# Kernel tuning notes

Hardware: AMD Instinct MI355X
Metric: run time of the kernel (lower is better)

## Reference

```python
import jax, jax.numpy as jnp
import numpy as np
from jax import lax

D_MODEL = 96
EXPAND = 2.66
D_INNER = int(EXPAND * D_MODEL)  # 255
DT_RANK = -(-D_MODEL // 16)      # 6
D_STATE = 8
K = 4                            # 4 scan directions
WIN = 8
NCLUST = 16
B, H, W = 2, 64, 64
N = H * W
L = 2 * N                        # opt/sar interleaved


def setup_inputs() -> dict:
    key = jax.random.key(0)
    ks = jax.random.split(key, 16)
    s = 0.05
    def rn(i, shape):
        return jax.random.normal(ks[i], shape, jnp.float32) * s
    # dt bias init: inv-softplus of dt ~ LogUniform[1e-3, 1e-1]
    dt = jnp.exp(jax.random.uniform(ks[10], (K, D_INNER)) * (np.log(0.1) - np.log(0.001)) + np.log(0.001))
    dt = jnp.clip(dt, 1e-4, None)
    inv_dt = dt + jnp.log(-jnp.expm1(-dt))
    A_logs = jnp.log(jnp.tile(jnp.arange(1, D_STATE + 1, dtype=jnp.float32)[None, :], (K * D_INNER, 1)))
    return dict(
        optical=jax.random.normal(ks[0], (B, D_MODEL, H, W), jnp.float32),
        sar=jax.random.normal(ks[1], (B, D_MODEL, H, W), jnp.float32),
        anchor_idx=jax.random.randint(ks[2], (B, NCLUST), 0, N),
        in_w_opt=rn(3, (2 * D_INNER, D_MODEL)),
        in_w_sar=rn(4, (2 * D_INNER, D_MODEL)),
        conv_w_opt=rn(5, (D_INNER, 1, 3, 3)),
        conv_b_opt=rn(6, (D_INNER,)),
        conv_w_sar=rn(7, (D_INNER, 1, 3, 3)),
        conv_b_sar=rn(8, (D_INNER,)),
        x_proj_weight=rn(9, (K, DT_RANK + 2 * D_STATE, D_INNER)),
        dt_projs_weight=rn(11, (K, D_INNER, DT_RANK)),
        dt_projs_bias=inv_dt.astype(jnp.float32),
        A_logs=A_logs,
        Ds=jnp.ones((K * D_INNER,), jnp.float32),
        ln_w_opt=jnp.ones((D_INNER,), jnp.float32),
        ln_b_opt=jnp.zeros((D_INNER,), jnp.float32),
        ln_w_sar=jnp.ones((D_INNER,), jnp.float32),
        ln_b_sar=jnp.zeros((D_INNER,), jnp.float32),
        out_w_opt=rn(12, (D_MODEL, D_INNER)),
        out_w_sar=rn(13, (D_MODEL, D_INNER)),
    )


def _dwconv(x, w, b):
    # depthwise 3x3, SAME padding; x: (B, D_INNER, H, W), w: (D_INNER, 1, 3, 3)
    y = lax.conv_general_dilated(x, w, (1, 1), [(1, 1), (1, 1)],
                                 dimension_numbers=('NCHW', 'OIHW', 'NCHW'),
                                 feature_group_count=D_INNER)
    return y + b[None, :, None, None]


def _ln(x, w, b):
    m = jnp.mean(x, -1, keepdims=True)
    v = jnp.mean((x - m) ** 2, -1, keepdims=True)
    return (x - m) * lax.rsqrt(v + 1e-5) * w + b


def _patches(x, order):
    # x: (B, C, H, W) -> (B, C, N) in one of 4 window-scan orders
    b, c, h, w_ = x.shape
    p = x.reshape(b, c, h // WIN, WIN, w_ // WIN, WIN)
    if order in ('ltr_utd', 'rtl_dtu'):
        p = p.transpose(0, 1, 2, 4, 3, 5)
    else:
        p = p.transpose(0, 1, 4, 2, 5, 3)
    if order in ('rtl_dtu', 'dtu_rtl'):
        p = jnp.flip(p, (2, 3, 4, 5))
    return p.reshape(b, c, -1)


def _selective_scan(u, delta, A, Bm, Cm, Ds2, bias):
    # u, delta: (B,K,C,L); A: (K,C,Ns); Bm, Cm: (B,K,Ns,L); Ds2, bias: (K,C)
    delta = jax.nn.softplus(delta + bias[None, :, :, None])
    u_l = jnp.moveaxis(u, 3, 0)      # (L,B,K,C)
    d_l = jnp.moveaxis(delta, 3, 0)
    B_l = jnp.moveaxis(Bm, 3, 0)     # (L,B,K,Ns)
    C_l = jnp.moveaxis(Cm, 3, 0)
    h0 = jnp.zeros(u.shape[:3] + (A.shape[-1],), u.dtype)  # (B,K,C,Ns)
    def step(h, inp):
        ut, dt, bt, ct = inp
        h = h * jnp.exp(dt[..., None] * A) + (dt * ut)[..., None] * bt[:, :, None, :]
        y = jnp.einsum('bkcn,bkn->bkc', h, ct)
        return h, y
    _, ys = lax.scan(step, h0, (u_l, d_l, B_l, C_l))
    return jnp.moveaxis(ys, 0, 3) + u * Ds2[None, :, :, None]


def _forward(optical, sar, in_w_opt, in_w_sar, conv_w_opt, conv_b_opt, conv_w_sar,
             conv_b_sar, x_proj_weight, dt_projs_weight, dt_projs_bias, A_logs, Ds,
             ln_w_opt, ln_b_opt, ln_w_sar, ln_b_sar, out_w_opt, out_w_sar, anchor_idx):
    C = D_INNER
    x_opt = optical.transpose(0, 2, 3, 1)  # (B,H,W,D_MODEL)
    x_sar = sar.transpose(0, 2, 3, 1)
    xo, zo = jnp.split(x_opt @ in_w_opt.T, 2, axis=-1)
    xs_, zs = jnp.split(x_sar @ in_w_sar.T, 2, axis=-1)
    xo = jax.nn.silu(_dwconv(xo.transpose(0, 3, 1, 2), conv_w_opt, conv_b_opt))   # (B,C,H,W)
    xs_ = jax.nn.silu(_dwconv(xs_.transpose(0, 3, 1, 2), conv_w_sar, conv_b_sar))
    # --- cluster-sorted token reorder ---
    xof = xo.reshape(B, C, N).transpose(0, 2, 1)   # (B,N,C)
    xsf = xs_.reshape(B, C, N).transpose(0, 2, 1)
    anchors = jnp.take_along_axis(xof, jnp.broadcast_to(anchor_idx[:, :, None], (B, NCLUST, C)), axis=1)
    d2 = (jnp.sum(xof ** 2, -1)[:, :, None] + jnp.sum(anchors ** 2, -1)[:, None, :]
          - 2.0 * jnp.einsum('bnc,bmc->bnm', xof, anchors))
    assign = jnp.argmin(d2, axis=2)            # (B,N)
    sorted_idx = jnp.argsort(assign, axis=1)
    inv_idx = jnp.argsort(sorted_idx, axis=1)
    go = jnp.take_along_axis(xof, jnp.broadcast_to(sorted_idx[:, :, None], xof.shape), 1).transpose(0, 2, 1).reshape(B, C, H, W)
    gs = jnp.take_along_axis(xsf, jnp.broadcast_to(sorted_idx[:, :, None], xsf.shape), 1).transpose(0, 2, 1).reshape(B, C, H, W)
    # --- 4-direction window scans, opt/sar interleaved ---
    seqs = []
    for order in ('ltr_utd', 'rtl_dtu', 'utd_ltr', 'dtu_rtl'):
        po = _patches(go, order)
        ps = _patches(gs, order)
        seqs.append(jnp.stack([po, ps], axis=-1).reshape(B, C, L))
    xs4 = jnp.stack(seqs, axis=1)  # (B,K,C,L)
    x_dbl = jnp.einsum('bkdl,kcd->bkcl', xs4, x_proj_weight)
    dts, Bs, Cs = jnp.split(x_dbl, [DT_RANK, DT_RANK + D_STATE], axis=2)
    dts = jnp.einsum('bkrl,kdr->bkdl', dts, dt_projs_weight)
    A = -jnp.exp(A_logs).reshape(K, D_INNER, D_STATE)
    out_y = _selective_scan(xs4, dts, A, Bs, Cs, Ds.reshape(K, D_INNER), dt_projs_bias)  # (B,K,C,L)
    y = jnp.sum(out_y, axis=1)                 # (B,C,L)
    yo = y[:, :, 0::2] / K                     # (B,C,N)
    ysr = y[:, :, 1::2] / K
    yo = jnp.take_along_axis(yo, jnp.broadcast_to(inv_idx[:, None, :], yo.shape), 2)
    ysr = jnp.take_along_axis(ysr, jnp.broadcast_to(inv_idx[:, None, :], ysr.shape), 2)
    yo = yo.transpose(0, 2, 1).reshape(B, H, W, C)
    ysr = ysr.transpose(0, 2, 1).reshape(B, H, W, C)
    yo = _ln(yo, ln_w_opt, ln_b_opt) * jax.nn.silu(zo)
    ysr = _ln(ysr, ln_w_sar, ln_b_sar) * jax.nn.silu(zs)
    out_opt = (yo @ out_w_opt.T).transpose(0, 3, 1, 2)
    out_sar = (ysr @ out_w_sar.T).transpose(0, 3, 1, 2)
    return out_opt, out_sar


def reference(optical, sar, in_w_opt, in_w_sar, conv_w_opt, conv_b_opt, conv_w_sar,
              conv_b_sar, x_proj_weight, dt_projs_weight, dt_projs_bias, A_logs, Ds,
              ln_w_opt, ln_b_opt, ln_w_sar, ln_b_sar, out_w_opt, out_w_sar, anchor_idx):
    return _forward(optical, sar, in_w_opt, in_w_sar, conv_w_opt, conv_b_opt, conv_w_sar,
                    conv_b_sar, x_proj_weight, dt_projs_weight, dt_projs_bias, A_logs, Ds,
                    ln_w_opt, ln_b_opt, ln_w_sar, ln_b_sar, out_w_opt, out_w_sar, anchor_idx)
```

## Files before the change

kernel.cpp:

```cpp
#include <hip/hip_runtime.h>
#include <math.h>

#define DM 96
#define DI 255
#define GSTR 256
#define NS 8
#define RK 6
#define NK 4
#define NB 2
#define NT 4096
#define LL 8192
#define NCL 16
#define GRP 16
#define NCH 512
#define NG (NCH / GRP)
#define CLN (NT / NCH)
#define XDS 96

__device__ __forceinline__ float sigm(float x) { return 1.f / (1.f + __expf(-x)); }

__global__ __launch_bounds__(256) void k_inproj(
    const float* __restrict__ opt, const float* __restrict__ sar,
    const float* __restrict__ w_o, const float* __restrict__ w_s,
    float* __restrict__ xpre_o, float* __restrict__ xpre_s,
    float* __restrict__ sz_o, float* __restrict__ sz_s)
{
  int tile = blockIdx.x;
  int oc = blockIdx.y & 1, m = blockIdx.y >> 1;
  int b = blockIdx.z;
  const float* inp = m ? sar : opt;
  const float* W   = m ? w_s : w_o;
  float* xp        = m ? xpre_s : xpre_o;
  float* szp       = m ? sz_s : sz_o;
  int n0 = tile * 64, c0 = oc * 256;
  __shared__ float xin[96 * 68];
  __shared__ float Wl[48 * 260];
  int tid = threadIdx.x;
  for (int idx = tid; idx < 96 * 64; idx += 256) {
    int d = idx >> 6, tk = idx & 63;
    xin[d * 68 + tk] = inp[(size_t)(b * DM + d) * NT + n0 + tk];
  }
  int tokg = tid & 7, og = tid >> 3;
  int tok0 = tokg * 8, o0 = og * 8;
  float acc[8][8];
#pragma unroll
  for (int j = 0; j < 8; ++j)
#pragma unroll
    for (int t = 0; t < 8; ++t) acc[j][t] = 0.f;
  for (int ks = 0; ks < 2; ++ks) {
    __syncthreads();
    {
      int row = c0 + tid; if (row > 509) row = 509;
      const float4* wg = (const float4*)(W + (size_t)row * 96 + ks * 48);
#pragma unroll
      for (int q = 0; q < 12; ++q) {
        float4 v = wg[q];
        Wl[(q * 4 + 0) * 260 + tid] = v.x;
        Wl[(q * 4 + 1) * 260 + tid] = v.y;
        Wl[(q * 4 + 2) * 260 + tid] = v.z;
        Wl[(q * 4 + 3) * 260 + tid] = v.w;
      }
    }
    __syncthreads();
    for (int dd = 0; dd < 48; ++dd) {
      int d = ks * 48 + dd;
      float4 xa = *(const float4*)&xin[d * 68 + tok0];
      float4 xb = *(const float4*)&xin[d * 68 + tok0 + 4];
      float4 wa = *(const float4*)&Wl[dd * 260 + o0];
      float4 wb = *(const float4*)&Wl[dd * 260 + o0 + 4];
      float xs8[8] = {xa.x, xa.y, xa.z, xa.w, xb.x, xb.y, xb.z, xb.w};
      float ws8[8] = {wa.x, wa.y, wa.z, wa.w, wb.x, wb.y, wb.z, wb.w};
#pragma unroll
      for (int j = 0; j < 8; ++j)
#pragma unroll
        for (int t = 0; t < 8; ++t) acc[j][t] = fmaf(ws8[j], xs8[t], acc[j][t]);
    }
  }
#pragma unroll
  for (int j = 0; j < 8; ++j) {
    int oo = c0 + o0 + j;
    if (oo < DI) {
      float4 v0 = make_float4(acc[j][0], acc[j][1], acc[j][2], acc[j][3]);
      float4 v1 = make_float4(acc[j][4], acc[j][5], acc[j][6], acc[j][7]);
      float* dst = xp + ((size_t)b * DI + oo) * NT + n0 + tok0;
      *(float4*)dst = v0;
      *(float4*)(dst + 4) = v1;
    } else if (oo < 510) {
      int cz = oo - DI;
#pragma unroll
      for (int t = 0; t < 8; ++t) {
        float v = acc[j][t];
        szp[((size_t)b * NT + n0 + tok0 + t) * GSTR + cz] = v * sigm(v);
      }
    }
  }
}

__global__ __launch_bounds__(256) void k_conv(
    const float* __restrict__ xpre_o, const float* __restrict__ xpre_s,
    const float* __restrict__ cw_o, const float* __restrict__ cb_o,
    const float* __restrict__ cw_s, const float* __restrict__ cb_s,
    float* __restrict__ G_o, float* __restrict__ G_s)
{
  int h = blockIdx.x & 63, cg = blockIdx.x >> 6;
  int m = blockIdx.y, b = blockIdx.z;
  const float* xp = m ? xpre_s : xpre_o;
  const float* cw = m ? cw_s : cw_o;
  const float* cb = m ? cb_s : cb_o;
  float* G = m ? G_s : G_o;
  int c0 = cg * 64;
  __shared__ float wts[64 * 9];
  __shared__ float bia[64];
  __shared__ float ot[64 * 65];
  int tid = threadIdx.x;
  for (int i = tid; i < 64 * 9; i += 256) {
    int c = c0 + i / 9;
    wts[i] = (c < DI) ? cw[c * 9 + i % 9] : 0.f;
  }
  if (tid < 64) bia[tid] = (c0 + tid < DI) ? cb[c0 + tid] : 0.f;
  __syncthreads();
  int w = tid & 63, g = tid >> 6;
  for (int t = 0; t < 16; ++t) {
    int ci = g * 16 + t;
    int c = c0 + ci;
    float a = bia[ci];
    if (c < DI) {
      const float* pl = xp + ((size_t)b * DI + c) * NT;
#pragma unroll
      for (int dh = -1; dh <= 1; ++dh) {
        int hh = h + dh;
        if (hh < 0 || hh >= 64) continue;
#pragma unroll
        for (int dw = -1; dw <= 1; ++dw) {
          int w2 = w + dw;
          if (w2 < 0 || w2 >= 64) continue;
          a = fmaf(pl[hh * 64 + w2], wts[ci * 9 + (dh + 1) * 3 + (dw + 1)], a);
        }
      }
    }
    ot[ci * 65 + w] = a * sigm(a);
  }
  __syncthreads();
  int c = c0 + w;
  if (c < DI) {
    for (int jj = 0; jj < 16; ++jj) {
      int j = g * 16 + jj;
      G[((size_t)b * NT + h * 64 + j) * GSTR + c] = ot[w * 65 + j];
    }
  } else if (c == DI) {
    for (int jj = 0; jj < 16; ++jj) {
      int j = g * 16 + jj;
      G[((size_t)b * NT + h * 64 + j) * GSTR + c] = 0.f;
    }
  }
}

__global__ __launch_bounds__(256) void k_cluster(
    const float* __restrict__ G_o, const int* __restrict__ aidx,
    int* __restrict__ assign)
{
  int tile = blockIdx.x, b = blockIdx.y;
  __shared__ float anch[NCL * 260];
  __shared__ float anrm[NCL];
  int tid = threadIdx.x;
  for (int idx = tid; idx < NCL * 256; idx += 256) {
    int mm = idx >> 8, c = idx & 255;
    anch[mm * 260 + c] = (c < DI)
        ? G_o[((size_t)b * NT + aidx[b * NCL + mm]) * GSTR + c] : 0.f;
  }
  __syncthreads();
  if (tid < NCL) {
    float s = 0.f;
    for (int c = 0; c < DI; ++c) { float v = anch[tid * 260 + c]; s = fmaf(v, v, s); }
    anrm[tid] = s;
  }
  __syncthreads();
  int lane = tid & 63, wv = tid >> 6;
  int mm = lane & 15, tg = lane >> 4;
  for (int p = 0; p < 2; ++p) {
    int n = tile * 32 + p * 16 + wv * 4 + tg;
    const float* row = G_o + ((size_t)b * NT + n) * GSTR;
    float dot = 0.f;
#pragma unroll 8
    for (int cb = 0; cb < 64; ++cb) {
      float4 x4 = *(const float4*)(row + cb * 4);
      float4 a4 = *(const float4*)&anch[mm * 260 + cb * 4];
      dot = fmaf(x4.x, a4.x, dot);
      dot = fmaf(x4.y, a4.y, dot);
      dot = fmaf(x4.z, a4.z, dot);
      dot = fmaf(x4.w, a4.w, dot);
    }
    float score = anrm[mm] - 2.f * dot;
    int bi = mm;
#pragma unroll
    for (int off = 1; off < 16; off <<= 1) {
      float os = __shfl_xor(score, off, 64);
      int oi = __shfl_xor(bi, off, 64);
      if (os < score || (os == score && oi < bi)) { score = os; bi = oi; }
    }
    if (mm == 0) assign[b * NT + n] = bi;
  }
}

__global__ __launch_bounds__(256) void k_sort(
    const int* __restrict__ assign, int* __restrict__ sorted,
    int* __restrict__ inv)
{
  int b = blockIdx.x;
  __shared__ int cnt[NCL];
  __shared__ int base[NCL];
  __shared__ int wcnt[4][NCL];
  int tid = threadIdx.x;
  if (tid < NCL) cnt[tid] = 0;
  __syncthreads();
  for (int ch = 0; ch < 16; ++ch) atomicAdd(&cnt[assign[b * NT + ch * 256 + tid]], 1);
  __syncthreads();
  if (tid == 0) {
    int run = 0;
    for (int mm = 0; mm < NCL; ++mm) { base[mm] = run; run += cnt[mm]; }
  }
  __syncthreads();
  int lane = tid & 63, wv = tid >> 6;
  for (int ch = 0; ch < 16; ++ch) {
    int n = ch * 256 + tid;
    int a = assign[b * NT + n];
    unsigned long long mymask = 0;
    for (int mm = 0; mm < NCL; ++mm) {
      unsigned long long msk = __ballot(a == mm);
      if (a == mm) mymask = msk;
      if (lane == mm) wcnt[wv][mm] = __popcll(msk);
    }
    __syncthreads();
    int before = 0;
    for (int w2 = 0; w2 < 4; ++w2) if (w2 < wv) before += wcnt[w2][a];
    before += __popcll(mymask & ((1ull << lane) - 1ull));
    int pos = base[a] + before;
    sorted[b * NT + pos] = n;
    inv[b * NT + n] = pos;
    __syncthreads();
    if (tid < NCL) base[tid] += wcnt[0][tid] + wcnt[1][tid] + wcnt[2][tid] + wcnt[3][tid];
    __syncthreads();
  }
}

__global__ __launch_bounds__(256) void k_stok(
    const int* __restrict__ sorted, int* __restrict__ stok)
{
  int idx = blockIdx.x * 256 + threadIdx.x;
  int n = idx & (NT - 1);
  int k = (idx >> 12) & 3;
  int b = idx >> 14;
  int nn = (k & 1) ? (NT - 1 - n) : n;
  int tok;
  if (k < 2) {
    int hb = (nn >> 9) & 7, wb = (nn >> 6) & 7, hi = (nn >> 3) & 7, wi = nn & 7;
    tok = ((hb << 3) + hi) * 64 + (wb << 3) + wi;
  } else {
    int wb = (nn >> 9) & 7, hb = (nn >> 6) & 7, wi = (nn >> 3) & 7, hi = nn & 7;
    tok = ((hb << 3) + hi) * 64 + (wb << 3) + wi;
  }
  stok[idx] = sorted[b * NT + tok];
}

__global__ __launch_bounds__(256) void k_wpad(
    const float* __restrict__ xpw, float* __restrict__ wpad)
{
  int row = blockIdx.x;
  int c = threadIdx.x;
  wpad[row * 256 + c] = (c < DI) ? xpw[row * DI + c] : 0.f;
}

__global__ __launch_bounds__(256) void k_xdbl(
    const float* __restrict__ G_o, const float* __restrict__ G_s,
    const float* __restrict__ wpad, float* __restrict__ xdbl)
{
  int tile = blockIdx.x, m = blockIdx.y, b = blockIdx.z;
  int j0 = tile * 32;
  __shared__ float xt[32 * 260];
  int tid = threadIdx.x;
  const float* G = m ? G_s : G_o;
  {
    const float4* src = (const float4*)(G + ((size_t)b * NT + j0) * GSTR);
    for (int i = tid; i < 32 * 64; i += 256) {
      int row = i >> 6, cq = i & 63;
      *(float4*)&xt[row * 260 + cq * 4] = src[i];
    }
  }
  __syncthreads();
  int ll = tid & 31, rq = tid >> 5;
  bool has2 = (rq < 6);
  float* orow = xdbl + ((size_t)((b * 2 + m) * NT) + j0 + ll) * XDS;
  const float* xr = &xt[ll * 260];
  for (int k = 0; k < NK; ++k) {
    const float* w0 = wpad + (k * 22 + rq) * 256;
    const float* w1 = wpad + (k * 22 + rq + 8) * 256;
    const float* w2 = wpad + (k * 22 + (has2 ? rq + 16 : rq)) * 256;
    float a0 = 0.f, a1 = 0.f, a2 = 0.f;
#pragma unroll 8
    for (int c4 = 0; c4 < 64; ++c4) {
      float4 x4 = *(const float4*)(xr + c4 * 4);
      float4 u0 = *(const float4*)(w0 + c4 * 4);
      float4 u1 = *(const float4*)(w1 + c4 * 4);
      float4 u2 = *(const float4*)(w2 + c4 * 4);
      a0 = fmaf(x4.x, u0.x, a0); a0 = fmaf(x4.y, u0.y, a0);
      a0 = fmaf(x4.z, u0.z, a0); a0 = fmaf(x4.w, u0.w, a0);
      a1 = fmaf(x4.x, u1.x, a1); a1 = fmaf(x4.y, u1.y, a1);
      a1 = fmaf(x4.z, u1.z, a1); a1 = fmaf(x4.w, u1.w, a1);
      a2 = fmaf(x4.x, u2.x, a2); a2 = fmaf(x4.y, u2.y, a2);
      a2 = fmaf(x4.z, u2.z, a2); a2 = fmaf(x4.w, u2.w, a2);
    }
    float* o = orow + k * 24;
    o[rq] = a0;
    o[rq + 8] = a1;
    if (has2) o[rq + 16] = a2;
  }
}

__global__ __launch_bounds__(256) void k_scan1(
    const float* __restrict__ G_o, const float* __restrict__ G_s,
    const int* __restrict__ stok, const float* __restrict__ xdbl,
    const float* __restrict__ dtw, const float* __restrict__ dtb,
    float* __restrict__ summ)
{
  int ch = blockIdx.x, k = blockIdx.y, b = blockIdx.z;
  int tid = threadIdx.x;
  int c = tid < DI ? tid : DI - 1;
  bool act = tid < DI;
  int rc = k * DI + c;
  float wdt[RK];
#pragma unroll
  for (int r = 0; r < RK; ++r) wdt[r] = dtw[rc * RK + r];
  float bias = dtb[rc];
  float st[NS];
#pragma unroll
  for (int nn = 0; nn < NS; ++nn) st[nn] = 0.f;
  float S = 0.f;
  int n0 = ch * CLN;
  const int* stk = stok + ((b * NK + k) << 12);
  int j = stk[n0];
  float u0 = G_o[((size_t)b * NT + j) * GSTR + c];
  float u1 = G_s[((size_t)b * NT + j) * GSTR + c];
  for (int ni = 0; ni < CLN; ++ni) {
    int j2 = 0; float u0n = 0.f, u1n = 0.f;
    if (ni + 1 < CLN) {
      j2 = stk[n0 + ni + 1];
      u0n = G_o[((size_t)b * NT + j2) * GSTR + c];
      u1n = G_s[((size_t)b * NT + j2) * GSTR + c];
    }
#pragma unroll
    for (int m = 0; m < 2; ++m) {
      const float* base = xdbl + ((size_t)((b * 2 + m) * NT) + j) * XDS + k * 24;
      float4 v0 = *(const float4*)(base);
      float4 v1 = *(const float4*)(base + 4);
      float4 v2 = *(const float4*)(base + 8);
      float4 v3 = *(const float4*)(base + 12);
      float draw = bias;
      draw = fmaf(v0.x, wdt[0], draw); draw = fmaf(v0.y, wdt[1], draw);
      draw = fmaf(v0.z, wdt[2], draw); draw = fmaf(v0.w, wdt[3], draw);
      draw = fmaf(v1.x, wdt[4], draw); draw = fmaf(v1.y, wdt[5], draw);
      float dlt = fmaxf(draw, 0.f) + __logf(1.f + __expf(-fabsf(draw)));
      S += dlt;
      float e1 = __expf(-dlt);
      float u = m ? u1 : u0;
      float du = dlt * u;
      float e2 = e1 * e1, e3 = e2 * e1, e4 = e2 * e2;
      float e5 = e4 * e1, e6 = e4 * e2, e7 = e6 * e1, e8 = e4 * e4;
      float p8[NS] = {e1, e2, e3, e4, e5, e6, e7, e8};
      float Bv[NS] = {v1.z, v1.w, v2.x, v2.y, v2.z, v2.w, v3.x, v3.y};
#pragma unroll
      for (int nn = 0; nn < NS; ++nn)
        st[nn] = fmaf(st[nn], p8[nn], du * Bv[nn]);
    }
    j = j2; u0 = u0n; u1 = u1n;
  }
  if (act) {
    size_t bb = (((size_t)b * NCH + ch) * NK + k) * 9;
#pragma unroll
    for (int nn = 0; nn < NS; ++nn) summ[(bb + nn) * DI + c] = st[nn];
    summ[(bb + 8) * DI + c] = S;
  }
}

__global__ __launch_bounds__(256) void k_scan3(
    const float* __restrict__ G_o, const float* __restrict__ G_s,
    const int* __restrict__ stok, const float* __restrict__ xdbl,
    const float* __restrict__ dtw, const float* __restrict__ dtb,
    const float* __restrict__ Dsp, const float* __restrict__ hst,
    float* __restrict__ Ya_o, float* __restrict__ Ya_s,
    float* __restrict__ Yb_o, float* __restrict__ Yb_s)
{
  int ch = blockIdx.x, kg = blockIdx.y, b = blockIdx.z;
  int k0 = kg * 2;
  int tid = threadIdx.x;
  int c = tid < DI ? tid : DI - 1;
  bool act = tid < DI;
  float* Yo = kg ? Yb_o : Ya_o;
  float* Ys = kg ? Yb_s : Ya_s;
  float wdt[2][RK], bias[2], dd[2], st[2][NS];
#pragma unroll
  for (int kk = 0; kk < 2; ++kk) {
    int rc = (k0 + kk) * DI + c;
#pragma unroll
    for (int r = 0; r < RK; ++r) wdt[kk][r] = dtw[rc * RK + r];
    bias[kk] = dtb[rc];
    dd[kk] = Dsp[rc];
#pragma unroll
    for (int nn = 0; nn < NS; ++nn)
      st[kk][nn] = hst[((((size_t)b * NCH + ch) * NK + k0 + kk) * NS + nn) * DI + c];
  }
  int n0 = ch * CLN;
  int jk[2];
  float u[2][2];
#pragma unroll
  for (int kk = 0; kk < 2; ++kk) jk[kk] = stok[((b * NK + k0 + kk) << 12) + n0];
#pragma unroll
  for (int m = 0; m < 2; ++m) {
    const float* G = m ? G_s : G_o;
#pragma unroll
    for (int kk = 0; kk < 2; ++kk) u[m][kk] = G[((size_t)b * NT + jk[kk]) * GSTR + c];
  }
  for (int ni = 0; ni < CLN; ++ni) {
    int n = n0 + ni;
    int jk2[2];
    float u2[2][2];
    if (ni + 1 < CLN) {
#pragma unroll
      for (int kk = 0; kk < 2; ++kk) jk2[kk] = stok[((b * NK + k0 + kk) << 12) + n + 1];
#pragma unroll
      for (int m = 0; m < 2; ++m) {
        const float* G = m ? G_s : G_o;
#pragma unroll
        for (int kk = 0; kk < 2; ++kk) u2[m][kk] = G[((size_t)b * NT + jk2[kk]) * GSTR + c];
      }
    }
#pragma unroll
    for (int m = 0; m < 2; ++m) {
      float ys = 0.f;
#pragma unroll
      for (int kk = 0; kk < 2; ++kk) {
        const float* base = xdbl + ((size_t)((b * 2 + m) * NT) + jk[kk]) * XDS + (k0 + kk) * 24;
        float4 v0 = *(const float4*)(base);
        float4 v1 = *(const float4*)(base + 4);
        float4 v2 = *(const float4*)(base + 8);
        float4 v3 = *(const float4*)(base + 12);
        float4 v4 = *(const float4*)(base + 16);
        float4 v5 = *(const float4*)(base + 20);
        float draw = bias[kk];
        draw = fmaf(v0.x, wdt[kk][0], draw); draw = fmaf(v0.y, wdt[kk][1], draw);
        draw = fmaf(v0.z, wdt[kk][2], draw); draw = fmaf(v0.w, wdt[kk][3], draw);
        draw = fmaf(v1.x, wdt[kk][4], draw); draw = fmaf(v1.y, wdt[kk][5], draw);
        float dlt = fmaxf(draw, 0.f) + __logf(1.f + __expf(-fabsf(draw)));
        float e1 = __expf(-dlt);
        float du = dlt * u[m][kk];
        float e2 = e1 * e1, e3 = e2 * e1, e4 = e2 * e2;
        float e5 = e4 * e1, e6 = e4 * e2, e7 = e6 * e1, e8 = e4 * e4;
        float p8[NS] = {e1, e2, e3, e4, e5, e6, e7, e8};
        float Bv[NS] = {v1.z, v1.w, v2.x, v2.y, v2.z, v2.w, v3.x, v3.y};
        float Cv[NS] = {v3.z, v3.w, v4.x, v4.y, v4.z, v4.w, v5.x, v5.y};
        float yk = 0.f;
#pragma unroll
        for (int nn = 0; nn < NS; ++nn) {
          st[kk][nn] = fmaf(st[kk][nn], p8[nn], du * Bv[nn]);
          yk = fmaf(st[kk][nn], Cv[nn], yk);
        }
        ys += yk + u[m][kk] * dd[kk];
      }
      if (act) {
        float* Y = m ? Ys : Yo;
        Y[((size_t)b * NT + n) * GSTR + c] = 0.25f * ys;
      }
    }
    if (ni + 1 < CLN) {
#pragma unroll
      for (int kk = 0; kk < 2; ++kk) jk[kk] = jk2[kk];
#pragma unroll
      for (int m = 0; m < 2; ++m)
#pragma unroll
        for (int kk = 0; kk < 2; ++kk) u[m][kk] = u2[m][kk];
    }
  }
}

__global__ __launch_bounds__(256) void k_comb_a(
    const float* __restrict__ summ, float* __restrict__ Aagg,
    float* __restrict__ Qagg)
{
  int g = blockIdx.x, yb = blockIdx.y;
  int nn = yb & 7, k = (yb >> 3) & 3, b = yb >> 5;
  int tid = threadIdx.x;
  int c = tid < DI ? tid : DI - 1;
  float fn = (float)(nn + 1);
  int ch0 = g * GRP;
  float q[GRP], S[GRP];
#pragma unroll
  for (int j = 0; j < GRP; ++j) {
    size_t bb = (((size_t)b * NCH + ch0 + j) * NK + k) * 9;
    q[j] = summ[(bb + nn) * DI + c];
    S[j] = summ[(bb + 8) * DI + c];
  }
  float A = 1.f, Q = 0.f;
#pragma unroll
  for (int j = 0; j < GRP; ++j) {
    float a = __expf(-S[j] * fn);
    Q = fmaf(a, Q, q[j]);
    A *= a;
  }
  if (tid < DI) {
    Aagg[((size_t)yb * NG + g) * DI + c] = A;
    Qagg[((size_t)yb * NG + g) * DI + c] = Q;
  }
}

__global__ __launch_bounds__(256) void k_comb_b(
    const float* __restrict__ Aagg, const float* __restrict__ Qagg,
    float* __restrict__ Hgrp)
{
  int yb = blockIdx.x;
  int tid = threadIdx.x;
  int c = tid < DI ? tid : DI - 1;
  bool act = tid < DI;
  float Av[NG], Qv[NG];
#pragma unroll
  for (int g = 0; g < NG; ++g) {
    Av[g] = Aagg[((size_t)yb * NG + g) * DI + c];
    Qv[g] = Qagg[((size_t)yb * NG + g) * DI + c];
  }
  float H = 0.f;
#pragma unroll
  for (int g = 0; g < NG; ++g) {
    if (act) Hgrp[((size_t)yb * NG + g) * DI + c] = H;
    H = fmaf(Av[g], H, Qv[g]);
  }
}

__global__ __launch_bounds__(256) void k_comb_c(
    const float* __restrict__ summ, const float* __restrict__ Hgrp,
    float* __restrict__ hst)
{
  int g = blockIdx.x, yb = blockIdx.y;
  int nn = yb & 7, k = (yb >> 3) & 3, b = yb >> 5;
  int tid = threadIdx.x;
  int c = tid < DI ? tid : DI - 1;
  bool act = tid < DI;
  float fn = (float)(nn + 1);
  int ch0 = g * GRP;
  float q[GRP], S[GRP];
#pragma unroll
  for (int j = 0; j < GRP; ++j) {
    size_t bb = (((size_t)b * NCH + ch0 + j) * NK + k) * 9;
    q[j] = summ[(bb + nn) * DI + c];
    S[j] = summ[(bb + 8) * DI + c];
  }
  float h = Hgrp[((size_t)yb * NG + g) * DI + c];
#pragma unroll
  for (int j = 0; j < GRP; ++j) {
    if (act)
      hst[((((size_t)b * NCH + ch0 + j) * NK + k) * NS + nn) * DI + c] = h;
    float a = __expf(-S[j] * fn);
    h = fmaf(a, h, q[j]);
  }
}

__global__ __launch_bounds__(256) void k_final(
    const float* __restrict__ Ya_o, const float* __restrict__ Ya_s,
    const float* __restrict__ Yb_o, const float* __restrict__ Yb_s,
    const int* __restrict__ inv,
    const float* __restrict__ sz_o, const float* __restrict__ sz_s,
    const float* __restrict__ lnw_o, const float* __restrict__ lnb_o,
    const float* __restrict__ lnw_s, const float* __restrict__ lnb_s,
    const float* __restrict__ ow_o, const float* __restrict__ ow_s,
    float* __restrict__ out)
{
  int tile = blockIdx.x, m = blockIdx.y, b = blockIdx.z;
  const float* Ya  = m ? Ya_s : Ya_o;
  const float* Yb  = m ? Yb_s : Yb_o;
  const float* szp = m ? sz_s : sz_o;
  const float* lnw = m ? lnw_s : lnw_o;
  const float* lnb = m ? lnb_s : lnb_o;
  const float* Wo  = m ? ow_s : ow_o;
  float* outp = out + ((size_t)m * NB + b) * DM * NT;
  int n0 = tile * 32;
  __shared__ float gt[256 * 36];
  __shared__ float Wl[64 * 98];
  int tid = threadIdx.x;
  int lane = tid & 63, wv = tid >> 6;
  float lnwv[4], lnbv[4];
#pragma unroll
  for (int q = 0; q < 4; ++q) {
    int c = lane + 64 * q;
    lnwv[q] = (c < DI) ? lnw[c] : 0.f;
    lnbv[q] = (c < DI) ? lnb[c] : 0.f;
  }
  for (int t = 0; t < 8; ++t) {
    int tok = wv * 8 + t;
    int r = inv[b * NT + n0 + tok];
    const float* yra = Ya + ((size_t)b * NT + r) * GSTR;
    const float* yrb = Yb + ((size_t)b * NT + r) * GSTR;
    const float* zr = szp + ((size_t)b * NT + n0 + tok) * GSTR;
    float yv[4], zv[4];
#pragma unroll
    for (int q = 0; q < 4; ++q) {
      int c = lane + 64 * q;
      bool ok = (c < DI);
      yv[q] = ok ? (yra[c] + yrb[c]) : 0.f;
      zv[q] = ok ? zr[c] : 0.f;
    }
    float s1 = yv[0] + yv[1] + yv[2] + yv[3];
    float s2 = yv[0] * yv[0] + yv[1] * yv[1] + yv[2] * yv[2] + yv[3] * yv[3];
#pragma unroll
    for (int o = 1; o < 64; o <<= 1) {
      s1 += __shfl_xor(s1, o, 64);
      s2 += __shfl_xor(s2, o, 64);
    }
    float mean = s1 * (1.f / DI);
    float var = s2 * (1.f / DI) - mean * mean;
    float rstd = rsqrtf(var + 1e-5f);
#pragma unroll
    for (int q = 0; q < 4; ++q) {
      int c = lane + 64 * q;
      float g = (c < DI) ? ((yv[q] - mean) * rstd * lnwv[q] + lnbv[q]) * zv[q] : 0.f;
      gt[c * 36 + tok] = g;
    }
  }
  int tokg = tid & 7, dg = tid >> 3;
  int t0 = tokg * 4, d0 = dg * 3;
  float acc[3][4];
#pragma unroll
  for (int j = 0; j < 3; ++j)
#pragma unroll
    for (int t = 0; t < 4; ++t) acc[j][t] = 0.f;
  for (int cc0 = 0; cc0 < 256; cc0 += 64) {
    __syncthreads();
    for (int i = tid; i < 96 * 64; i += 256) {
      int d = i >> 6, cl = i & 63;
      int c = cc0 + cl;
      Wl[cl * 98 + d] = (c < DI) ? Wo[d * DI + c] : 0.f;
    }
    __syncthreads();
    for (int cl = 0; cl < 64; ++cl) {
      float4 g4 = *(const float4*)&gt[(cc0 + cl) * 36 + t0];
      const float* wr = &Wl[cl * 98 + d0];
      float w0 = wr[0], w1 = wr[1], w2 = wr[2];
      float gv[4] = {g4.x, g4.y, g4.z, g4.w};
#pragma unroll
      for (int t = 0; t < 4; ++t) {
        acc[0][t] = fmaf(w0, gv[t], acc[0][t]);
        acc[1][t] = fmaf(w1, gv[t], acc[1][t]);
        acc[2][t] = fmaf(w2, gv[t], acc[2][t]);
      }
    }
  }
#pragma unroll
  for (int j = 0; j < 3; ++j) {
    float4 v = make_float4(acc[j][0], acc[j][1], acc[j][2], acc[j][3]);
    *(float4*)(outp + (size_t)(d0 + j) * NT + n0 + t0) = v;
  }
}

extern "C" void kernel_launch(void* const* d_in, const int* in_sizes, int n_in,
                              void* d_out, int out_size, void* d_ws, size_t ws_size,
                              hipStream_t stream)
{
  (void)in_sizes; (void)n_in; (void)out_size; (void)ws_size;
  const float* opt    = (const float*)d_in[0];
  const float* sar    = (const float*)d_in[1];
  const int*   aidx   = (const int*)d_in[2];
  const float* w_in_o = (const float*)d_in[3];
  const float* w_in_s = (const float*)d_in[4];
  const float* cw_o   = (const float*)d_in[5];
  const float* cb_o   = (const float*)d_in[6];
  const float* cw_s   = (const float*)d_in[7];
  const float* cb_s   = (const float*)d_in[8];
  const float* xpw    = (const float*)d_in[9];
  const float* dtw    = (const float*)d_in[10];
  const float* dtb    = (const float*)d_in[11];
  const float* Dsp    = (const float*)d_in[13];
  const float* lnw_o  = (const float*)d_in[14];
  const float* lnb_o  = (const float*)d_in[15];
  const float* lnw_s  = (const float*)d_in[16];
  const float* lnb_s  = (const float*)d_in[17];
  const float* ow_o   = (const float*)d_in[18];
  const float* ow_s   = (const float*)d_in[19];
  float* out = (float*)d_out;

  char* wsb = (char*)d_ws;
  size_t off = 0;
  auto take = [&](size_t nbytes) {
    char* p = wsb + off;
    off += (nbytes + 255) & ~(size_t)255;
    return p;
  };
  float* xpre_o = (float*)take(sizeof(float) * (size_t)NB * NT * GSTR);
  float* xpre_s = (float*)take(sizeof(float) * (size_t)NB * NT * GSTR);
  float* G_o    = (float*)take(sizeof(float) * (size_t)NB * NT * GSTR);
  float* G_s    = (float*)take(sizeof(float) * (size_t)NB * NT * GSTR);
  float* sz_o   = (float*)take(sizeof(float) * (size_t)NB * NT * GSTR);
  float* sz_s   = (float*)take(sizeof(float) * (size_t)NB * NT * GSTR);
  float* xdbl   = (float*)take(sizeof(float) * (size_t)NB * 2 * NT * XDS);
  float* wpad   = (float*)take(sizeof(float) * 88 * 256);
  int* assign   = (int*)take(sizeof(int) * NB * NT);
  int* sorted   = (int*)take(sizeof(int) * NB * NT);
  int* invp     = (int*)take(sizeof(int) * NB * NT);
  int* stok     = (int*)take(sizeof(int) * NB * NK * NT);
  float* summ = (float*)take(sizeof(float) * (size_t)NB * NCH * NK * 9 * DI);
  float* hst  = (float*)take(sizeof(float) * (size_t)NB * NCH * NK * NS * DI);
  float* Aagg = (float*)take(sizeof(float) * (size_t)64 * NG * DI);
  float* Qagg = (float*)take(sizeof(float) * (size_t)64 * NG * DI);
  float* Hgrp = (float*)take(sizeof(float) * (size_t)64 * NG * DI);
  float* Ya_o = xpre_o;
  float* Ya_s = xpre_s;
  float* Yb_o = summ;
  float* Yb_s = summ + (size_t)NB * NT * GSTR;

  k_wpad<<<88, 256, 0, stream>>>(xpw, wpad);
  k_inproj<<<dim3(64, 4, NB), 256, 0, stream>>>(opt, sar, w_in_o, w_in_s,
                                                xpre_o, xpre_s, sz_o, sz_s);
  k_conv<<<dim3(256, 2, NB), 256, 0, stream>>>(xpre_o, xpre_s, cw_o, cb_o, cw_s, cb_s, G_o, G_s);
  k_cluster<<<dim3(128, NB), 256, 0, stream>>>(G_o, aidx, assign);
  k_sort<<<NB, 256, 0, stream>>>(assign, sorted, invp);
  k_stok<<<NB * NK * 16, 256, 0, stream>>>(sorted, stok);
  k_xdbl<<<dim3(128, 2, NB), 256, 0, stream>>>(G_o, G_s, wpad, xdbl);
  k_scan1<<<dim3(NCH, NK, NB), 256, 0, stream>>>(G_o, G_s, stok, xdbl, dtw, dtb, summ);
  k_comb_a<<<dim3(NG, 64), 256, 0, stream>>>(summ, Aagg, Qagg);
  k_comb_b<<<64, 256, 0, stream>>>(Aagg, Qagg, Hgrp);
  k_comb_c<<<dim3(NG, 64), 256, 0, stream>>>(summ, Hgrp, hst);
  k_scan3<<<dim3(NCH, 2, NB), 256, 0, stream>>>(G_o, G_s, stok, xdbl, dtw, dtb,
                                                Dsp, hst, Ya_o, Ya_s, Yb_o, Yb_s);
  k_final<<<dim3(128, 2, NB), 256, 0, stream>>>(Ya_o, Ya_s, Yb_o, Yb_s, invp, sz_o, sz_s,
                                                lnw_o, lnb_o, lnw_s, lnb_s, ow_o, ow_s, out);
}
```

Measured before the change: 295.6 us.

## Stage scan inputs in shared memory, pair reversed directions, retile x_proj

k_scan1 now handles a forward/reverse direction pair per block. It relies on the reversed direction's token order being the mirror of the forward one, so it loads the tokens, x_dbl rows and u values for a chunk once and reuses them for both directions. k_scan3 also prefetches its chunk's tokens, x_dbl slices and u values into shared memory and registers up front, replacing the per-step dependent global loads. k_xdbl is retiled to 8 tokens per block, with each thread computing up to three of the 88 output features in one pass instead of looping over directions. This trades more registers (u arrays of CLN entries) and extra syncs for fewer scattered, latency-bound loads, and it depends on the reverse-order symmetry of the token lists holding.

```diff
diff --git a/kernel.cpp b/kernel.cpp
--- a/kernel.cpp
+++ b/kernel.cpp
@@ -275,45 +275,43 @@
     const float* __restrict__ wpad, float* __restrict__ xdbl)
 {
   int tile = blockIdx.x, m = blockIdx.y, b = blockIdx.z;
-  int j0 = tile * 32;
-  __shared__ float xt[32 * 260];
+  int j0 = tile * 8;
+  __shared__ float xt[8 * 260];
   int tid = threadIdx.x;
   const float* G = m ? G_s : G_o;
   {
     const float4* src = (const float4*)(G + ((size_t)b * NT + j0) * GSTR);
-    for (int i = tid; i < 32 * 64; i += 256) {
+    for (int i = tid; i < 8 * 64; i += 256) {
       int row = i >> 6, cq = i & 63;
       *(float4*)&xt[row * 260 + cq * 4] = src[i];
     }
   }
   __syncthreads();
-  int ll = tid & 31, rq = tid >> 5;
-  bool has2 = (rq < 6);
+  int ll = tid & 7, rg = tid >> 3;
+  int f0 = rg, f1 = rg + 32, f2 = rg + 64;
+  bool has2 = (rg < 24);
+  const float* w0 = wpad + f0 * 256;
+  const float* w1 = wpad + f1 * 256;
+  const float* w2 = wpad + (has2 ? f2 : f0) * 256;
+  const float* xr = &xt[ll * 260];
+  float a0 = 0.f, a1 = 0.f, a2 = 0.f;
+#pragma unroll 8
+  for (int c4 = 0; c4 < 64; ++c4) {
+    float4 x4 = *(const float4*)(xr + c4 * 4);
+    float4 u0 = *(const float4*)(w0 + c4 * 4);
+    float4 u1 = *(const float4*)(w1 + c4 * 4);
+    float4 u2 = *(const float4*)(w2 + c4 * 4);
+    a0 = fmaf(x4.x, u0.x, a0); a0 = fmaf(x4.y, u0.y, a0);
+    a0 = fmaf(x4.z, u0.z, a0); a0 = fmaf(x4.w, u0.w, a0);
+    a1 = fmaf(x4.x, u1.x, a1); a1 = fmaf(x4.y, u1.y, a1);
+    a1 = fmaf(x4.z, u1.z, a1); a1 = fmaf(x4.w, u1.w, a1);
+    a2 = fmaf(x4.x, u2.x, a2); a2 = fmaf(x4.y, u2.y, a2);
+    a2 = fmaf(x4.z, u2.z, a2); a2 = fmaf(x4.w, u2.w, a2);
+  }
   float* orow = xdbl + ((size_t)((b * 2 + m) * NT) + j0 + ll) * XDS;
-  const float* xr = &xt[ll * 260];
-  for (int k = 0; k < NK; ++k) {
-    const float* w0 = wpad + (k * 22 + rq) * 256;
-    const float* w1 = wpad + (k * 22 + rq + 8) * 256;
-    const float* w2 = wpad + (k * 22 + (has2 ? rq + 16 : rq)) * 256;
-    float a0 = 0.f, a1 = 0.f, a2 = 0.f;
-#pragma unroll 8
-    for (int c4 = 0; c4 < 64; ++c4) {
-      float4 x4 = *(const float4*)(xr + c4 * 4);
-      float4 u0 = *(const float4*)(w0 + c4 * 4);
-      float4 u1 = *(const float4*)(w1 + c4 * 4);
-      float4 u2 = *(const float4*)(w2 + c4 * 4);
-      a0 = fmaf(x4.x, u0.x, a0); a0 = fmaf(x4.y, u0.y, a0);
-      a0 = fmaf(x4.z, u0.z, a0); a0 = fmaf(x4.w, u0.w, a0);
-      a1 = fmaf(x4.x, u1.x, a1); a1 = fmaf(x4.y, u1.y, a1);
-      a1 = fmaf(x4.z, u1.z, a1); a1 = fmaf(x4.w, u1.w, a1);
-      a2 = fmaf(x4.x, u2.x, a2); a2 = fmaf(x4.y, u2.y, a2);
-      a2 = fmaf(x4.z, u2.z, a2); a2 = fmaf(x4.w, u2.w, a2);
-    }
-    float* o = orow + k * 24;
-    o[rq] = a0;
-    o[rq + 8] = a1;
-    if (has2) o[rq + 16] = a2;
-  }
+  orow[(f0 / 22) * 24 + (f0 % 22)] = a0;
+  orow[(f1 / 22) * 24 + (f1 % 22)] = a1;
+  if (has2) orow[(f2 / 22) * 24 + (f2 % 22)] = a2;
 }
 
 __global__ __launch_bounds__(256) void k_scan1(
@@ -322,62 +320,69 @@
     const float* __restrict__ dtw, const float* __restrict__ dtb,
     float* __restrict__ summ)
 {
-  int ch = blockIdx.x, k = blockIdx.y, b = blockIdx.z;
+  int ch = blockIdx.x, p = blockIdx.y, b = blockIdx.z;
+  int k0 = 2 * p, k1 = 2 * p + 1;
   int tid = threadIdx.x;
   int c = tid < DI ? tid : DI - 1;
   bool act = tid < DI;
-  int rc = k * DI + c;
-  float wdt[RK];
-#pragma unroll
-  for (int r = 0; r < RK; ++r) wdt[r] = dtw[rc * RK + r];
-  float bias = dtb[rc];
-  float st[NS];
-#pragma unroll
-  for (int nn = 0; nn < NS; ++nn) st[nn] = 0.f;
-  float S = 0.f;
-  int n0 = ch * CLN;
-  const int* stk = stok + ((b * NK + k) << 12);
-  int j = stk[n0];
-  float u0 = G_o[((size_t)b * NT + j) * GSTR + c];
-  float u1 = G_s[((size_t)b * NT + j) * GSTR + c];
-  for (int ni = 0; ni < CLN; ++ni) {
-    int j2 = 0; float u0n = 0.f, u1n = 0.f;
-    if (ni + 1 < CLN) {
-      j2 = stk[n0 + ni + 1];
-      u0n = G_o[((size_t)b * NT + j2) * GSTR + c];
-      u1n = G_s[((size_t)b * NT + j2) * GSTR + c];
-    }
-#pragma unroll
-    for (int m = 0; m < 2; ++m) {
-      const float* base = xdbl + ((size_t)((b * 2 + m) * NT) + j) * XDS + k * 24;
-      float4 v0 = *(const float4*)(base);
-      float4 v1 = *(const float4*)(base + 4);
-      float4 v2 = *(const float4*)(base + 8);
-      float4 v3 = *(const float4*)(base + 12);
-      float draw = bias;
-      draw = fmaf(v0.x, wdt[0], draw); draw = fmaf(v0.y, wdt[1], draw);
-      draw = fmaf(v0.z, wdt[2], draw); draw = fmaf(v0.w, wdt[3], draw);
-      draw = fmaf(v1.x, wdt[4], draw); draw = fmaf(v1.y, wdt[5], draw);
-      float dlt = fmaxf(draw, 0.f) + __logf(1.f + __expf(-fabsf(draw)));
-      S += dlt;
-      float e1 = __expf(-dlt);
-      float u = m ? u1 : u0;
-      float du = dlt * u;
-      float e2 = e1 * e1, e3 = e2 * e1, e4 = e2 * e2;
-      float e5 = e4 * e1, e6 = e4 * e2, e7 = e6 * e1, e8 = e4 * e4;
-      float p8[NS] = {e1, e2, e3, e4, e5, e6, e7, e8};
-      float Bv[NS] = {v1.z, v1.w, v2.x, v2.y, v2.z, v2.w, v3.x, v3.y};
-#pragma unroll
-      for (int nn = 0; nn < NS; ++nn)
-        st[nn] = fmaf(st[nn], p8[nn], du * Bv[nn]);
-    }
-    j = j2; u0 = u0n; u1 = u1n;
-  }
-  if (act) {
-    size_t bb = (((size_t)b * NCH + ch) * NK + k) * 9;
-#pragma unroll
-    for (int nn = 0; nn < NS; ++nn) summ[(bb + nn) * DI + c] = st[nn];
-    summ[(bb + 8) * DI + c] = S;
+  __shared__ int toks[CLN];
+  __shared__ float xds[2][CLN][48];
+  if (tid < CLN) toks[tid] = stok[((b * NK + k0) << 12) + ch * CLN + tid];
+  __syncthreads();
+  for (int i = tid; i < 2 * CLN * 48; i += 256) {
+    int m = i / (CLN * 48), rem = i % (CLN * 48);
+    int st_ = rem / 48, q = rem % 48;
+    xds[m][st_][q] = xdbl[((size_t)((b * 2 + m) * NT) + toks[st_]) * XDS + p * 48 + q];
+  }
+  float u[2][CLN];
+#pragma unroll
+  for (int i = 0; i < CLN; ++i) {
+    u[0][i] = G_o[((size_t)b * NT + toks[i]) * GSTR + c];
+    u[1][i] = G_s[((size_t)b * NT + toks[i]) * GSTR + c];
+  }
+  float wdt[2][RK], bias[2];
+#pragma unroll
+  for (int kk = 0; kk < 2; ++kk) {
+    int rc = (k0 + kk) * DI + c;
+#pragma unroll
+    for (int r = 0; r < RK; ++r) wdt[kk][r] = dtw[rc * RK + r];
+    bias[kk] = dtb[rc];
+  }
+  __syncthreads();
+#pragma unroll
+  for (int kk = 0; kk < 2; ++kk) {
+    float st[NS];
+#pragma unroll
+    for (int nn = 0; nn < NS; ++nn) st[nn] = 0.f;
+    float S = 0.f;
+    for (int i = 0; i < CLN; ++i) {
+      int step = kk ? (CLN - 1 - i) : i;
+      int xoff = kk ? 24 : 0;
+#pragma unroll
+      for (int m = 0; m < 2; ++m) {
+        const float* xd = &xds[m][step][xoff];
+        float draw = bias[kk];
+#pragma unroll
+        for (int r = 0; r < RK; ++r) draw = fmaf(xd[r], wdt[kk][r], draw);
+        float dlt = fmaxf(draw, 0.f) + __logf(1.f + __expf(-fabsf(draw)));
+        S += dlt;
+        float e1 = __expf(-dlt);
+        float du = dlt * u[m][step];
+        float e2 = e1 * e1, e3 = e2 * e1, e4 = e2 * e2;
+        float e5 = e4 * e1, e6 = e4 * e2, e7 = e6 * e1, e8 = e4 * e4;
+        float p8[NS] = {e1, e2, e3, e4, e5, e6, e7, e8};
+#pragma unroll
+        for (int nn = 0; nn < NS; ++nn)
+          st[nn] = fmaf(st[nn], p8[nn], du * xd[6 + nn]);
+      }
+    }
+    if (act) {
+      int chs = kk ? (NCH - 1 - ch) : ch;
+      size_t bb = (((size_t)b * NCH + chs) * NK + k0 + kk) * 9;
+#pragma unroll
+      for (int nn = 0; nn < NS; ++nn) summ[(bb + nn) * DI + c] = st[nn];
+      summ[(bb + 8) * DI + c] = S;
+    }
   }
 }
 
@@ -390,12 +395,35 @@
     float* __restrict__ Yb_o, float* __restrict__ Yb_s)
 {
   int ch = blockIdx.x, kg = blockIdx.y, b = blockIdx.z;
-  int k0 = kg * 2;
+  int k0 = 2 * kg;
   int tid = threadIdx.x;
   int c = tid < DI ? tid : DI - 1;
   bool act = tid < DI;
   float* Yo = kg ? Yb_o : Ya_o;
   float* Ys = kg ? Yb_s : Ya_s;
+  __shared__ int tk[2][CLN];
+  __shared__ float xds[2][2][CLN][24];
+  if (tid < 2 * CLN) {
+    int kk = tid / CLN, i = tid % CLN;
+    tk[kk][i] = stok[((b * NK + k0 + kk) << 12) + ch * CLN + i];
+  }
+  __syncthreads();
+  for (int i = tid; i < 2 * 2 * CLN * 24; i += 256) {
+    int kk = i / (2 * CLN * 24), r1 = i % (2 * CLN * 24);
+    int m = r1 / (CLN * 24), r2 = r1 % (CLN * 24);
+    int st_ = r2 / 24, q = r2 % 24;
+    xds[kk][m][st_][q] =
+        xdbl[((size_t)((b * 2 + m) * NT) + tk[kk][st_]) * XDS + (k0 + kk) * 24 + q];
+  }
+  float u[2][2][CLN];
+#pragma unroll
+  for (int i = 0; i < CLN; ++i) {
+#pragma unroll
+    for (int kk = 0; kk < 2; ++kk) {
+      u[0][kk][i] = G_o[((size_t)b * NT + tk[kk][i]) * GSTR + c];
+      u[1][kk][i] = G_s[((size_t)b * NT + tk[kk][i]) * GSTR + c];
+    }
+  }
   float wdt[2][RK], bias[2], dd[2], st[2][NS];
 #pragma unroll
   for (int kk = 0; kk < 2; ++kk) {
@@ -408,75 +436,36 @@
     for (int nn = 0; nn < NS; ++nn)
       st[kk][nn] = hst[((((size_t)b * NCH + ch) * NK + k0 + kk) * NS + nn) * DI + c];
   }
+  __syncthreads();
   int n0 = ch * CLN;
-  int jk[2];
-  float u[2][2];
-#pragma unroll
-  for (int kk = 0; kk < 2; ++kk) jk[kk] = stok[((b * NK + k0 + kk) << 12) + n0];
-#pragma unroll
-  for (int m = 0; m < 2; ++m) {
-    const float* G = m ? G_s : G_o;
-#pragma unroll
-    for (int kk = 0; kk < 2; ++kk) u[m][kk] = G[((size_t)b * NT + jk[kk]) * GSTR + c];
-  }
-  for (int ni = 0; ni < CLN; ++ni) {
-    int n = n0 + ni;
-    int jk2[2];
-    float u2[2][2];
-    if (ni + 1 < CLN) {
-#pragma unroll
-      for (int kk = 0; kk < 2; ++kk) jk2[kk] = stok[((b * NK + k0 + kk) << 12) + n + 1];
-#pragma unroll
-      for (int m = 0; m < 2; ++m) {
-        const float* G = m ? G_s : G_o;
-#pragma unroll
-        for (int kk = 0; kk < 2; ++kk) u2[m][kk] = G[((size_t)b * NT + jk2[kk]) * GSTR + c];
-      }
-    }
+  for (int i = 0; i < CLN; ++i) {
 #pragma unroll
     for (int m = 0; m < 2; ++m) {
       float ys = 0.f;
 #pragma unroll
       for (int kk = 0; kk < 2; ++kk) {
-        const float* base = xdbl + ((size_t)((b * 2 + m) * NT) + jk[kk]) * XDS + (k0 + kk) * 24;
-        float4 v0 = *(const float4*)(base);
-        float4 v1 = *(const float4*)(base + 4);
-        float4 v2 = *(const float4*)(base + 8);
-        float4 v3 = *(const float4*)(base + 12);
-        float4 v4 = *(const float4*)(base + 16);
-        float4 v5 = *(const float4*)(base + 20);
+        const float* xd = &xds[kk][m][i][0];
         float draw = bias[kk];
-        draw = fmaf(v0.x, wdt[kk][0], draw); draw = fmaf(v0.y, wdt[kk][1], draw);
-        draw = fmaf(v0.z, wdt[kk][2], draw); draw = fmaf(v0.w, wdt[kk][3], draw);
-        draw = fmaf(v1.x, wdt[kk][4], draw); draw = fmaf(v1.y, wdt[kk][5], draw);
+#pragma unroll
+        for (int r = 0; r < RK; ++r) draw = fmaf(xd[r], wdt[kk][r], draw);
         float dlt = fmaxf(draw, 0.f) + __logf(1.f + __expf(-fabsf(draw)));
         float e1 = __expf(-dlt);
-        float du = dlt * u[m][kk];
+        float du = dlt * u[m][kk][i];
         float e2 = e1 * e1, e3 = e2 * e1, e4 = e2 * e2;
         float e5 = e4 * e1, e6 = e4 * e2, e7 = e6 * e1, e8 = e4 * e4;
         float p8[NS] = {e1, e2, e3, e4, e5, e6, e7, e8};
-        float Bv[NS] = {v1.z, v1.w, v2.x, v2.y, v2.z, v2.w, v3.x, v3.y};
-        float Cv[NS] = {v3.z, v3.w, v4.x, v4.y, v4.z, v4.w, v5.x, v5.y};
         float yk = 0.f;
 #pragma unroll
         for (int nn = 0; nn < NS; ++nn) {
-          st[kk][nn] = fmaf(st[kk][nn], p8[nn], du * Bv[nn]);
-          yk = fmaf(st[kk][nn], Cv[nn], yk);
+          st[kk][nn] = fmaf(st[kk][nn], p8[nn], du * xd[6 + nn]);
+          yk = fmaf(st[kk][nn], xd[14 + nn], yk);
         }
-        ys += yk + u[m][kk] * dd[kk];
+        ys += yk + u[m][kk][i] * dd[kk];
       }
       if (act) {
         float* Y = m ? Ys : Yo;
-        Y[((size_t)b * NT + n) * GSTR + c] = 0.25f * ys;
+        Y[((size_t)b * NT + n0 + i) * GSTR + c] = 0.25f * ys;
       }
-    }
-    if (ni + 1 < CLN) {
-#pragma unroll
-      for (int kk = 0; kk < 2; ++kk) jk[kk] = jk2[kk];
-#pragma unroll
-      for (int m = 0; m < 2; ++m)
-#pragma unroll
-        for (int kk = 0; kk < 2; ++kk) u[m][kk] = u2[m][kk];
     }
   }
 }
@@ -719,8 +708,8 @@
   k_cluster<<<dim3(128, NB), 256, 0, stream>>>(G_o, aidx, assign);
   k_sort<<<NB, 256, 0, stream>>>(assign, sorted, invp);
   k_stok<<<NB * NK * 16, 256, 0, stream>>>(sorted, stok);
-  k_xdbl<<<dim3(128, 2, NB), 256, 0, stream>>>(G_o, G_s, wpad, xdbl);
-  k_scan1<<<dim3(NCH, NK, NB), 256, 0, stream>>>(G_o, G_s, stok, xdbl, dtw, dtb, summ);
+  k_xdbl<<<dim3(512, 2, NB), 256, 0, stream>>>(G_o, G_s, wpad, xdbl);
+  k_scan1<<<dim3(NCH, 2, NB), 256, 0, stream>>>(G_o, G_s, stok, xdbl, dtw, dtb, summ);
   k_comb_a<<<dim3(NG, 64), 256, 0, stream>>>(summ, Aagg, Qagg);
   k_comb_b<<<64, 256, 0, stream>>>(Aagg, Qagg, Hgrp);
   k_comb_c<<<dim3(NG, 64), 256, 0, stream>>>(summ, Hgrp, hst);
```

After: 290.7 us. No clear change (-1.7%).
